# Kernel optimization log

Measured on AMD Instinct MI355X. Metric: run time of the kernel, lower is better.

The kernel has to match this reference:

```python
import jax, jax.numpy as jnp
import numpy as np

DIM = 2048
MEM = 64
EPS = 1e-5


def setup_inputs() -> dict:
    key = jax.random.key(0)
    ks = jax.random.split(key, 6)
    x = jax.random.normal(ks[0], (8, 4096, DIM), dtype=jnp.float32)
    memory_slots = jax.random.normal(ks[1], (MEM, DIM), dtype=jnp.float32) * 0.02
    # memory_gate: Linear(dim -> memory_size)
    Wg = jax.random.normal(ks[2], (DIM, MEM), dtype=jnp.float32) / np.sqrt(DIM)
    bg = jnp.zeros((MEM,), dtype=jnp.float32)
    # memory_update: Linear(2*dim -> dim)
    Wu = jax.random.normal(ks[3], (2 * DIM, DIM), dtype=jnp.float32) / np.sqrt(2 * DIM)
    bu = jnp.zeros((DIM,), dtype=jnp.float32)
    gamma = jnp.ones((DIM,), dtype=jnp.float32)
    beta = jnp.zeros((DIM,), dtype=jnp.float32)
    return {"x": x, "memory_slots": memory_slots, "Wg": Wg, "bg": bg,
            "Wu": Wu, "bu": bu, "gamma": gamma, "beta": beta}


def _layer_norm(h, gamma, beta):
    mu = jnp.mean(h, axis=-1, keepdims=True)
    var = jnp.mean(jnp.square(h - mu), axis=-1, keepdims=True)
    return (h - mu) * jax.lax.rsqrt(var + EPS) * gamma + beta


def reference(x, memory_slots, Wg, bg, Wu, bu, gamma, beta):
    # gates: [B, S, M]
    memory_gates = jax.nn.sigmoid(jnp.einsum('bsd,dm->bsm', x, Wg) + bg)
    # retrieval: [B, S, D]
    memory_retrieved = jnp.einsum('bsm,md->bsd', memory_gates, memory_slots)
    combined = jnp.concatenate([x, memory_retrieved], axis=-1)  # [B, S, 2D]
    memory_enhanced = jnp.einsum('bse,ed->bsd', combined, Wu) + bu
    return _layer_norm(memory_enhanced, gamma, beta)
```

## Files before the change

kernel.cpp:

```cpp
#include <hip/hip_runtime.h>
#include <hip/hip_bf16.h>

typedef __bf16 bf16x8 __attribute__((ext_vector_type(8)));
typedef float f32x4 __attribute__((ext_vector_type(4)));
typedef float f32x16 __attribute__((ext_vector_type(16)));
typedef unsigned short u16;
typedef u16 u16x8 __attribute__((ext_vector_type(8)));

#define DIM 2048
#define MEM 64
#define KC 2112
#define MTOK 32768
#define BK 32
#define NT (KC/BK)

__device__ __forceinline__ u16 f2bf(float f) {
  union { float f; unsigned u; } v; v.f = f;
  unsigned r = v.u + 0x7FFF + ((v.u >> 16) & 1);
  return (u16)(r >> 16);
}
__device__ __forceinline__ float bf2f(u16 u) {
  union { unsigned u; float f; } v; v.u = ((unsigned)u) << 16; return v.f;
}

#define GLDS16(g, l) __builtin_amdgcn_global_load_lds( \
    (const __attribute__((address_space(1))) void*)(g), \
    (__attribute__((address_space(3))) void*)(l), 16, 0, 0)

__global__ __launch_bounds__(256) void prep_wu1(const float* __restrict__ Wu,
                                                u16* __restrict__ WcatT) {
  __shared__ float tile[64][65];
  int bk = blockIdx.x & 31;
  int bn = blockIdx.x >> 5;
  int tx = threadIdx.x & 63, g = threadIdx.x >> 6;
#pragma unroll
  for (int i = 0; i < 16; ++i)
    tile[g + i*4][tx] = Wu[(size_t)(bk*64 + g + i*4)*DIM + bn*64 + tx];
  __syncthreads();
#pragma unroll
  for (int i = 0; i < 16; ++i) {
    int n = bn*64 + g + i*4;
    WcatT[(size_t)n*KC + bk*64 + tx] = f2bf(tile[tx][g + i*4]);
  }
}

__global__ __launch_bounds__(256) void prep_m2a(const float* __restrict__ ms,
                                                const float* __restrict__ Wu,
                                                float* __restrict__ M2p) {
  int n  = blockIdx.x*256 + threadIdx.x;
  int mg = blockIdx.y;
  int kc = blockIdx.z;
  const float* w2 = Wu + (size_t)DIM*DIM + n;
  const float* m0 = ms + (size_t)(mg*4+0)*DIM;
  const float* m1 = ms + (size_t)(mg*4+1)*DIM;
  const float* m2 = ms + (size_t)(mg*4+2)*DIM;
  const float* m3 = ms + (size_t)(mg*4+3)*DIM;
  float a0=0.f, a1=0.f, a2=0.f, a3=0.f;
  int d0 = kc*256;
  for (int d = d0; d < d0+256; ++d) {
    float w = w2[(size_t)d*DIM];
    a0 += m0[d]*w; a1 += m1[d]*w; a2 += m2[d]*w; a3 += m3[d]*w;
  }
  M2p[((size_t)kc*64 + mg*4 + 0)*2048 + n] = a0;
  M2p[((size_t)kc*64 + mg*4 + 1)*2048 + n] = a1;
  M2p[((size_t)kc*64 + mg*4 + 2)*2048 + n] = a2;
  M2p[((size_t)kc*64 + mg*4 + 3)*2048 + n] = a3;
}

__global__ __launch_bounds__(256) void prep_m2b(const float* __restrict__ M2p,
                                                u16* __restrict__ WcatT) {
  int i = blockIdx.x*256 + threadIdx.x;
  float s = 0.f;
#pragma unroll
  for (int kc = 0; kc < 8; ++kc) s += M2p[(size_t)kc*131072 + i];
  int m = i >> 11, n = i & 2047;
  WcatT[(size_t)n*KC + DIM + m] = f2bf(s);
}

__global__ __launch_bounds__(256) void prep_wg(const float* __restrict__ Wg,
                                               u16* __restrict__ WgT) {
  __shared__ float tile[64][65];
  int k0 = blockIdx.x * 64;
  int tx = threadIdx.x & 63, g = threadIdx.x >> 6;
#pragma unroll
  for (int i = 0; i < 16; ++i)
    tile[g + i*4][tx] = Wg[(size_t)(k0 + g + i*4)*MEM + tx];
  __syncthreads();
#pragma unroll
  for (int i = 0; i < 16; ++i) {
    int m = g + i*4;
    WgT[(size_t)m*DIM + k0 + tx] = f2bf(tile[tx][m]);
  }
}

__global__ __launch_bounds__(256) void conv_gates(const float* __restrict__ x,
                                                  const u16* __restrict__ WgT,
                                                  const float* __restrict__ bg,
                                                  u16* __restrict__ Acat) {
  __shared__ u16 As[64*32];
  __shared__ u16 Bs[64*32];
  const int brow = blockIdx.x;
  const int tid = threadIdx.x;
  const int w = tid >> 6, l = tid & 63;
  const int wm = w >> 1, wn = w & 1;
  const int lrow = l & 15, lk = l >> 4;

  const int r  = tid >> 2;
  const int cb = (tid & 3) * 8;
  const float* xp = x + (size_t)(brow*64 + r)*DIM + cb;
  u16* aout = Acat + (size_t)(brow*64 + r)*KC + cb;

  f32x4 acc[2][2] = {};
  const bf16x8* Al = reinterpret_cast<const bf16x8*>(As);
  const bf16x8* Bl = reinterpret_cast<const bf16x8*>(Bs);
  const int abase = (wm*32 + lrow)*4 + lk;
  const int bbase = (wn*32 + lrow)*4 + lk;

  float4 v0 = *reinterpret_cast<const float4*>(xp);
  float4 v1 = *reinterpret_cast<const float4*>(xp + 4);

  for (int k0 = 0; k0 < DIM; k0 += 32) {
    const u16* bgp = WgT + (size_t)(tid>>2)*DIM + k0 + (tid&3)*8;
    GLDS16(bgp, ((u16*)Bs) + tid*8);
    u16x8 o;
    o[0]=f2bf(v0.x); o[1]=f2bf(v0.y); o[2]=f2bf(v0.z); o[3]=f2bf(v0.w);
    o[4]=f2bf(v1.x); o[5]=f2bf(v1.y); o[6]=f2bf(v1.z); o[7]=f2bf(v1.w);
    const bool more = (k0 + 32 < DIM);
    if (more) {
      v0 = *reinterpret_cast<const float4*>(xp + k0 + 32);
      v1 = *reinterpret_cast<const float4*>(xp + k0 + 36);
    }
    __builtin_amdgcn_s_barrier();
    *reinterpret_cast<u16x8*>(As + tid*8) = o;
    *reinterpret_cast<u16x8*>(aout + k0) = o;
    if (more) { asm volatile("s_waitcnt vmcnt(3) lgkmcnt(0)" ::: "memory"); }
    else      { asm volatile("s_waitcnt vmcnt(1) lgkmcnt(0)" ::: "memory"); }
    __builtin_amdgcn_sched_barrier(0);
    __builtin_amdgcn_s_barrier();
    bf16x8 a0v = Al[abase], a1v = Al[abase + 64];
    bf16x8 b0v = Bl[bbase], b1v = Bl[bbase + 64];
    acc[0][0] = __builtin_amdgcn_mfma_f32_16x16x32_bf16(a0v, b0v, acc[0][0], 0, 0, 0);
    acc[0][1] = __builtin_amdgcn_mfma_f32_16x16x32_bf16(a0v, b1v, acc[0][1], 0, 0, 0);
    acc[1][0] = __builtin_amdgcn_mfma_f32_16x16x32_bf16(a1v, b0v, acc[1][0], 0, 0, 0);
    acc[1][1] = __builtin_amdgcn_mfma_f32_16x16x32_bf16(a1v, b1v, acc[1][1], 0, 0, 0);
  }

#pragma unroll
  for (int fn = 0; fn < 2; ++fn) {
    int c = wn*32 + fn*16 + lrow;
    float b = bg[c];
#pragma unroll
    for (int fm = 0; fm < 2; ++fm)
#pragma unroll
      for (int rg = 0; rg < 4; ++rg) {
        int t = brow*64 + wm*32 + fm*16 + lk*4 + rg;
        float logit = acc[fm][fn][rg] + b;
        float gv = 1.0f / (1.0f + __expf(-logit));
        Acat[(size_t)t*KC + DIM + c] = f2bf(gv);
      }
  }
}

__global__ __launch_bounds__(512, 2) void gemm_main8(const u16* __restrict__ A,
                                                     const u16* __restrict__ Bt,
                                                     const float* __restrict__ bu,
                                                     float* __restrict__ Hf,
                                                     u16* __restrict__ Hb) {
  __shared__ u16 AsB[4*8192];
  __shared__ u16 BsB[4*8192];

  const int bid = blockIdx.x;
  const int wg  = (bid & 7) * (int)(gridDim.x >> 3) + (bid >> 3);
  const int brow = wg >> 3;
  const int bcol = wg & 7;
  const int tid = threadIdx.x;
  const int w = tid >> 6, l = tid & 63;
  const int wm = w >> 2, wn = w & 3;
  const int l31 = l & 31, lr5 = l >> 5;

  const int xor5  = ((tid >> 5) & 1) << 5;
  const int kelem = (((tid & 3) * 16) ^ xor5) >> 1;
  const int rowst = tid >> 2;
  const u16* Asrc0 = A  + (size_t)(brow*256 + rowst)*KC + kelem;
  const u16* Asrc1 = A  + (size_t)(brow*256 + 128 + rowst)*KC + kelem;
  const u16* Bsrc0 = Bt + (size_t)(bcol*256 + rowst)*KC + kelem;
  const u16* Bsrc1 = Bt + (size_t)(bcol*256 + 128 + rowst)*KC + kelem;
  const int p0 = tid*16, p1 = 8192 + tid*16;
  char* AsC = (char*)AsB;
  char* BsC = (char*)BsB;

  int aoff[4][2], boff[2][2];
#pragma unroll
  for (int rf = 0; rf < 4; ++rf)
#pragma unroll
    for (int ks = 0; ks < 2; ++ks) {
      int row = wm*128 + rf*32 + l31;
      int lg  = row*64 + ks*32 + lr5*16;
      aoff[rf][ks] = lg ^ (((row >> 3) & 1) << 5);
    }
#pragma unroll
  for (int cf = 0; cf < 2; ++cf)
#pragma unroll
    for (int ks = 0; ks < 2; ++ks) {
      int row = wn*64 + cf*32 + l31;
      int lg  = row*64 + ks*32 + lr5*16;
      boff[cf][ks] = lg ^ (((row >> 3) & 1) << 5);
    }

  f32x16 acc[4][2] = {};

#define STAGE_A(kt) { const int bb_ = ((kt)&3)*16384; \
    GLDS16(Asrc0 + (size_t)(kt)*BK, AsC + bb_ + p0); \
    GLDS16(Asrc1 + (size_t)(kt)*BK, AsC + bb_ + p1); }
#define STAGE_B(kt) { const int bb_ = ((kt)&3)*16384; \
    GLDS16(Bsrc0 + (size_t)(kt)*BK, BsC + bb_ + p0); \
    GLDS16(Bsrc1 + (size_t)(kt)*BK, BsC + bb_ + p1); }
#define MFMA32(av, bv, c) __builtin_amdgcn_mfma_f32_32x32x16_bf16(av, bv, c, 0, 0, 0)

  STAGE_A(0); STAGE_B(0);
  STAGE_A(1); STAGE_B(1);
  STAGE_A(2); STAGE_B(2);
  asm volatile("s_waitcnt vmcnt(8)" ::: "memory");
  __builtin_amdgcn_sched_barrier(0);
  __builtin_amdgcn_s_barrier();
  __builtin_amdgcn_sched_barrier(0);

#pragma unroll 1
  for (int t = 0; t < NT; ++t) {
    const char* Ab = AsC + (t & 3) * 16384;
    const char* Bb = BsC + (t & 3) * 16384;

    bf16x8 a0 = *(const bf16x8*)(Ab + aoff[0][0]);
    bf16x8 a1 = *(const bf16x8*)(Ab + aoff[1][0]);
    bf16x8 a2 = *(const bf16x8*)(Ab + aoff[2][0]);
    bf16x8 a3 = *(const bf16x8*)(Ab + aoff[3][0]);
    bf16x8 b0 = *(const bf16x8*)(Bb + boff[0][0]);
    bf16x8 b1 = *(const bf16x8*)(Bb + boff[1][0]);
    if (t + 3 < NT) STAGE_A(t + 3);
    __builtin_amdgcn_s_setprio(1);
    acc[0][0] = MFMA32(a0, b0, acc[0][0]);
    acc[0][1] = MFMA32(a0, b1, acc[0][1]);
    acc[1][0] = MFMA32(a1, b0, acc[1][0]);
    acc[1][1] = MFMA32(a1, b1, acc[1][1]);
    acc[2][0] = MFMA32(a2, b0, acc[2][0]);
    acc[2][1] = MFMA32(a2, b1, acc[2][1]);
    acc[3][0] = MFMA32(a3, b0, acc[3][0]);
    acc[3][1] = MFMA32(a3, b1, acc[3][1]);
    __builtin_amdgcn_s_setprio(0);

    bf16x8 a4 = *(const bf16x8*)(Ab + aoff[0][1]);
    bf16x8 a5 = *(const bf16x8*)(Ab + aoff[1][1]);
    bf16x8 a6 = *(const bf16x8*)(Ab + aoff[2][1]);
    bf16x8 a7 = *(const bf16x8*)(Ab + aoff[3][1]);
    bf16x8 b2 = *(const bf16x8*)(Bb + boff[0][1]);
    bf16x8 b3 = *(const bf16x8*)(Bb + boff[1][1]);
    if (t + 3 < NT) STAGE_B(t + 3);
    __builtin_amdgcn_s_setprio(1);
    acc[0][0] = MFMA32(a4, b2, acc[0][0]);
    acc[0][1] = MFMA32(a4, b3, acc[0][1]);
    acc[1][0] = MFMA32(a5, b2, acc[1][0]);
    acc[1][1] = MFMA32(a5, b3, acc[1][1]);
    acc[2][0] = MFMA32(a6, b2, acc[2][0]);
    acc[2][1] = MFMA32(a6, b3, acc[2][1]);
    acc[3][0] = MFMA32(a7, b2, acc[3][0]);
    acc[3][1] = MFMA32(a7, b3, acc[3][1]);
    __builtin_amdgcn_s_setprio(0);

    if (t <= NT-4)      { asm volatile("s_waitcnt vmcnt(8)" ::: "memory"); }
    else if (t == NT-3) { asm volatile("s_waitcnt vmcnt(4)" ::: "memory"); }
    else                { asm volatile("s_waitcnt vmcnt(0)" ::: "memory"); }
    __builtin_amdgcn_sched_barrier(0);
    __builtin_amdgcn_s_barrier();
    __builtin_amdgcn_sched_barrier(0);
  }
#undef STAGE_A
#undef STAGE_B
#undef MFMA32

  const int orow = brow*256 + wm*128;
  const int ocol = bcol*256 + wn*64;
  if (Hb) {
#pragma unroll
    for (int cf = 0; cf < 2; ++cf) {
      const int c = ocol + cf*32 + l31;
      const float bias = bu[c];
#pragma unroll
      for (int rf = 0; rf < 4; ++rf) {
        const int br = orow + rf*32 + 4*lr5;
#pragma unroll
        for (int reg = 0; reg < 16; ++reg) {
          const int row = br + (reg & 3) + 8*(reg >> 2);
          Hb[(size_t)row*DIM + c] = f2bf(acc[rf][cf][reg] + bias);
        }
      }
    }
  } else {
#pragma unroll
    for (int cf = 0; cf < 2; ++cf) {
      const int c = ocol + cf*32 + l31;
      const float bias = bu[c];
#pragma unroll
      for (int rf = 0; rf < 4; ++rf) {
        const int br = orow + rf*32 + 4*lr5;
#pragma unroll
        for (int reg = 0; reg < 16; ++reg) {
          const int row = br + (reg & 3) + 8*(reg >> 2);
          Hf[(size_t)row*DIM + c] = acc[rf][cf][reg] + bias;
        }
      }
    }
  }
}

__global__ __launch_bounds__(256) void ln_b(const u16* __restrict__ Hb,
                                            float* __restrict__ out,
                                            const float* __restrict__ gamma,
                                            const float* __restrict__ beta) {
  const int tid = threadIdx.x;
  const int c0 = tid*8;
  const int w = tid >> 6;
  __shared__ float ss[4], ss2[4];
  float g8[8], be8[8];
#pragma unroll
  for (int j = 0; j < 8; ++j) { g8[j] = gamma[c0+j]; be8[j] = beta[c0+j]; }

#pragma unroll
  for (int rr = 0; rr < 2; ++rr) {
    const int row = blockIdx.x*2 + rr;
    const u16* h = Hb + (size_t)row*DIM;
    u16x8 hv = *reinterpret_cast<const u16x8*>(h + c0);
    float v[8];
#pragma unroll
    for (int j = 0; j < 8; ++j) v[j] = bf2f(hv[j]);
    float s = 0.f, s2 = 0.f;
#pragma unroll
    for (int j = 0; j < 8; ++j) { s += v[j]; s2 += v[j]*v[j]; }
#pragma unroll
    for (int o = 32; o >= 1; o >>= 1) { s += __shfl_xor(s, o); s2 += __shfl_xor(s2, o); }
    if ((tid & 63) == 0) { ss[w] = s; ss2[w] = s2; }
    __syncthreads();
    s  = ss[0]+ss[1]+ss[2]+ss[3];
    s2 = ss2[0]+ss2[1]+ss2[2]+ss2[3];
    __syncthreads();
    float mu  = s * (1.0f/DIM);
    float var = s2 * (1.0f/DIM) - mu*mu;
    float rs  = rsqrtf(var + 1e-5f);
    float o8[8];
#pragma unroll
    for (int j = 0; j < 8; ++j) o8[j] = (v[j]-mu)*rs*g8[j] + be8[j];
    float4 oa = {o8[0],o8[1],o8[2],o8[3]}, ob = {o8[4],o8[5],o8[6],o8[7]};
    float* op = out + (size_t)row*DIM;
    reinterpret_cast<float4*>(op)[tid*2]   = oa;
    reinterpret_cast<float4*>(op)[tid*2+1] = ob;
  }
}

__global__ __launch_bounds__(256) void ln_inplace(float* __restrict__ H,
                                                  const float* __restrict__ gamma,
                                                  const float* __restrict__ beta) {
  int row = blockIdx.x;
  float* h = H + (size_t)row*DIM;
  int tid = threadIdx.x;
  float4 a = reinterpret_cast<const float4*>(h)[tid*2];
  float4 b = reinterpret_cast<const float4*>(h)[tid*2+1];
  float v[8] = {a.x,a.y,a.z,a.w,b.x,b.y,b.z,b.w};
  float s = 0.f, s2 = 0.f;
#pragma unroll
  for (int j = 0; j < 8; ++j) { s += v[j]; s2 += v[j]*v[j]; }
#pragma unroll
  for (int o = 32; o >= 1; o >>= 1) { s += __shfl_xor(s, o); s2 += __shfl_xor(s2, o); }
  __shared__ float ss[4], ss2[4];
  int w = tid >> 6;
  if ((tid & 63) == 0) { ss[w] = s; ss2[w] = s2; }
  __syncthreads();
  s  = ss[0]+ss[1]+ss[2]+ss[3];
  s2 = ss2[0]+ss2[1]+ss2[2]+ss2[3];
  float mu  = s * (1.0f/DIM);
  float var = s2 * (1.0f/DIM) - mu*mu;
  float rs  = rsqrtf(var + 1e-5f);
  int c0 = tid*8;
  float o8[8];
#pragma unroll
  for (int j = 0; j < 8; ++j) o8[j] = (v[j]-mu)*rs*gamma[c0+j] + beta[c0+j];
  float4 oa = {o8[0],o8[1],o8[2],o8[3]}, ob = {o8[4],o8[5],o8[6],o8[7]};
  reinterpret_cast<float4*>(h)[tid*2]   = oa;
  reinterpret_cast<float4*>(h)[tid*2+1] = ob;
}

extern "C" void kernel_launch(void* const* d_in, const int* in_sizes, int n_in,
                              void* d_out, int out_size, void* d_ws, size_t ws_size,
                              hipStream_t stream) {
  const float* x     = (const float*)d_in[0];
  const float* ms    = (const float*)d_in[1];
  const float* Wg    = (const float*)d_in[2];
  const float* bg    = (const float*)d_in[3];
  const float* Wu    = (const float*)d_in[4];
  const float* bu    = (const float*)d_in[5];
  const float* gamma = (const float*)d_in[6];
  const float* beta  = (const float*)d_in[7];
  float* out = (float*)d_out;

  char* wsp = (char*)d_ws;
  const size_t offAcat  = 0;
  const size_t offWcatT = offAcat  + (size_t)MTOK*KC*2;
  const size_t offWgT   = offWcatT + (size_t)DIM*KC*2;
  const size_t offHb    = offWgT   + (size_t)MEM*DIM*2;
  const size_t needHb   = offHb + (size_t)MTOK*DIM*2;

  u16* Acat  = (u16*)(wsp + offAcat);
  u16* WcatT = (u16*)(wsp + offWcatT);
  u16* WgT   = (u16*)(wsp + offWgT);
  float* M2p = (float*)wsp;
  u16* Hb    = (ws_size >= needHb) ? (u16*)(wsp + offHb) : nullptr;

  prep_m2a<<<dim3(8,16,8), 256, 0, stream>>>(ms, Wu, M2p);
  prep_m2b<<<512, 256, 0, stream>>>(M2p, WcatT);
  prep_wu1<<<1024, 256, 0, stream>>>(Wu, WcatT);
  prep_wg<<<32, 256, 0, stream>>>(Wg, WgT);
  conv_gates<<<512, 256, 0, stream>>>(x, WgT, bg, Acat);
  gemm_main8<<<1024, 512, 0, stream>>>(Acat, WcatT, bu, out, Hb);
  if (Hb) ln_b<<<16384, 256, 0, stream>>>(Hb, out, gamma, beta);
  else    ln_inplace<<<32768, 256, 0, stream>>>(out, gamma, beta);
}
```

Before: 533.2 us.

## Rework main GEMM to 16x16x32 MFMA with BK=64 double-buffered split-K pipeline

The main bf16 GEMM now uses 16x16x32 MFMA tiles instead of 32x32x16. Each iteration consumes 64 K-elements from a double buffer, split into two 32-wide halves, instead of 32 K-elements from a four-stage ring. Global-to-LDS staging of the next tile is interleaved with the MFMA groups using extra barriers and finer vmcnt waits, and the LDS swizzle and epilogue indexing change to match the new fragment layout. The aim is better overlap of loads with compute and fewer loop iterations. The cost is more barriers per iteration and a shallower prefetch depth.

```diff
diff --git a/kernel.cpp b/kernel.cpp
--- a/kernel.cpp
+++ b/kernel.cpp
@@ -3,7 +3,6 @@
 
 typedef __bf16 bf16x8 __attribute__((ext_vector_type(8)));
 typedef float f32x4 __attribute__((ext_vector_type(4)));
-typedef float f32x16 __attribute__((ext_vector_type(16)));
 typedef unsigned short u16;
 typedef u16 u16x8 __attribute__((ext_vector_type(8)));
 
@@ -11,8 +10,7 @@
 #define MEM 64
 #define KC 2112
 #define MTOK 32768
-#define BK 32
-#define NT (KC/BK)
+#define NT64 33
 
 __device__ __forceinline__ u16 f2bf(float f) {
   union { float f; unsigned u; } v; v.f = f;
@@ -166,8 +164,8 @@
                                                      const float* __restrict__ bu,
                                                      float* __restrict__ Hf,
                                                      u16* __restrict__ Hb) {
-  __shared__ u16 AsB[4*8192];
-  __shared__ u16 BsB[4*8192];
+  __shared__ u16 AsB[2*2*8192];
+  __shared__ u16 BsB[2*2*8192];
 
   const int bid = blockIdx.x;
   const int wg  = (bid & 7) * (int)(gridDim.x >> 3) + (bid >> 3);
@@ -176,137 +174,164 @@
   const int tid = threadIdx.x;
   const int w = tid >> 6, l = tid & 63;
   const int wm = w >> 2, wn = w & 3;
-  const int l31 = l & 31, lr5 = l >> 5;
-
-  const int xor5  = ((tid >> 5) & 1) << 5;
-  const int kelem = (((tid & 3) * 16) ^ xor5) >> 1;
-  const int rowst = tid >> 2;
-  const u16* Asrc0 = A  + (size_t)(brow*256 + rowst)*KC + kelem;
-  const u16* Asrc1 = A  + (size_t)(brow*256 + 128 + rowst)*KC + kelem;
-  const u16* Bsrc0 = Bt + (size_t)(bcol*256 + rowst)*KC + kelem;
-  const u16* Bsrc1 = Bt + (size_t)(bcol*256 + 128 + rowst)*KC + kelem;
-  const int p0 = tid*16, p1 = 8192 + tid*16;
+  const int l15 = l & 15, lk = l >> 4;
+
   char* AsC = (char*)AsB;
   char* BsC = (char*)BsB;
 
-  int aoff[4][2], boff[2][2];
-#pragma unroll
-  for (int rf = 0; rf < 4; ++rf)
-#pragma unroll
-    for (int ks = 0; ks < 2; ++ks) {
-      int row = wm*128 + rf*32 + l31;
-      int lg  = row*64 + ks*32 + lr5*16;
-      aoff[rf][ks] = lg ^ (((row >> 3) & 1) << 5);
-    }
-#pragma unroll
-  for (int cf = 0; cf < 2; ++cf)
-#pragma unroll
-    for (int ks = 0; ks < 2; ++ks) {
-      int row = wn*64 + cf*32 + l31;
-      int lg  = row*64 + ks*32 + lr5*16;
-      boff[cf][ks] = lg ^ (((row >> 3) & 1) << 5);
-    }
-
-  f32x16 acc[4][2] = {};
-
-#define STAGE_A(kt) { const int bb_ = ((kt)&3)*16384; \
-    GLDS16(Asrc0 + (size_t)(kt)*BK, AsC + bb_ + p0); \
-    GLDS16(Asrc1 + (size_t)(kt)*BK, AsC + bb_ + p1); }
-#define STAGE_B(kt) { const int bb_ = ((kt)&3)*16384; \
-    GLDS16(Bsrc0 + (size_t)(kt)*BK, BsC + bb_ + p0); \
-    GLDS16(Bsrc1 + (size_t)(kt)*BK, BsC + bb_ + p1); }
-#define MFMA32(av, bv, c) __builtin_amdgcn_mfma_f32_32x32x16_bf16(av, bv, c, 0, 0, 0)
-
-  STAGE_A(0); STAGE_B(0);
-  STAGE_A(1); STAGE_B(1);
-  STAGE_A(2); STAGE_B(2);
-  asm volatile("s_waitcnt vmcnt(8)" ::: "memory");
+  const int po0 = tid*16, po1 = 8192 + tid*16;
+  const int lo0 = po0 ^ (((po0 >> 9) & 1) << 5);
+  const int lo1 = po1 ^ (((po1 >> 9) & 1) << 5);
+  const int r0 = lo0 >> 6, k0e = (lo0 & 63) >> 1;
+  const int r1 = lo1 >> 6, k1e = (lo1 & 63) >> 1;
+  const u16* Ag0 = A  + (size_t)(brow*256 + r0)*KC + k0e;
+  const u16* Ag1 = A  + (size_t)(brow*256 + r1)*KC + k1e;
+  const u16* Bg0 = Bt + (size_t)(bcol*256 + r0)*KC + k0e;
+  const u16* Bg1 = Bt + (size_t)(bcol*256 + r1)*KC + k1e;
+
+  int aoff[8], boff[4];
+#pragma unroll
+  for (int rf = 0; rf < 8; ++rf) {
+    int row = wm*128 + rf*16 + l15;
+    int lg  = row*64 + lk*16;
+    aoff[rf] = lg ^ (((lg >> 9) & 1) << 5);
+  }
+#pragma unroll
+  for (int cf = 0; cf < 4; ++cf) {
+    int row = wn*64 + cf*16 + l15;
+    int lg  = row*64 + lk*16;
+    boff[cf] = lg ^ (((lg >> 9) & 1) << 5);
+  }
+
+  f32x4 acc[8][4] = {};
+
+#define STAGE_A_KH(kt, kh) { char* d_ = AsC + ((kt)&1)*32768 + (kh)*16384; \
+    GLDS16(Ag0 + (size_t)(kt)*64 + (kh)*32, d_ + po0); \
+    GLDS16(Ag1 + (size_t)(kt)*64 + (kh)*32, d_ + po1); }
+#define STAGE_B_KH(kt, kh) { char* d_ = BsC + ((kt)&1)*32768 + (kh)*16384; \
+    GLDS16(Bg0 + (size_t)(kt)*64 + (kh)*32, d_ + po0); \
+    GLDS16(Bg1 + (size_t)(kt)*64 + (kh)*32, d_ + po1); }
+#define MFMA16(av, bv, c) __builtin_amdgcn_mfma_f32_16x16x32_bf16(av, bv, c, 0, 0, 0)
+
+  STAGE_A_KH(0, 0); STAGE_B_KH(0, 0);
+  STAGE_A_KH(0, 1); STAGE_B_KH(0, 1);
+  asm volatile("s_waitcnt vmcnt(0)" ::: "memory");
   __builtin_amdgcn_sched_barrier(0);
   __builtin_amdgcn_s_barrier();
   __builtin_amdgcn_sched_barrier(0);
 
 #pragma unroll 1
-  for (int t = 0; t < NT; ++t) {
-    const char* Ab = AsC + (t & 3) * 16384;
-    const char* Bb = BsC + (t & 3) * 16384;
-
-    bf16x8 a0 = *(const bf16x8*)(Ab + aoff[0][0]);
-    bf16x8 a1 = *(const bf16x8*)(Ab + aoff[1][0]);
-    bf16x8 a2 = *(const bf16x8*)(Ab + aoff[2][0]);
-    bf16x8 a3 = *(const bf16x8*)(Ab + aoff[3][0]);
-    bf16x8 b0 = *(const bf16x8*)(Bb + boff[0][0]);
-    bf16x8 b1 = *(const bf16x8*)(Bb + boff[1][0]);
-    if (t + 3 < NT) STAGE_A(t + 3);
-    __builtin_amdgcn_s_setprio(1);
-    acc[0][0] = MFMA32(a0, b0, acc[0][0]);
-    acc[0][1] = MFMA32(a0, b1, acc[0][1]);
-    acc[1][0] = MFMA32(a1, b0, acc[1][0]);
-    acc[1][1] = MFMA32(a1, b1, acc[1][1]);
-    acc[2][0] = MFMA32(a2, b0, acc[2][0]);
-    acc[2][1] = MFMA32(a2, b1, acc[2][1]);
-    acc[3][0] = MFMA32(a3, b0, acc[3][0]);
-    acc[3][1] = MFMA32(a3, b1, acc[3][1]);
-    __builtin_amdgcn_s_setprio(0);
-
-    bf16x8 a4 = *(const bf16x8*)(Ab + aoff[0][1]);
-    bf16x8 a5 = *(const bf16x8*)(Ab + aoff[1][1]);
-    bf16x8 a6 = *(const bf16x8*)(Ab + aoff[2][1]);
-    bf16x8 a7 = *(const bf16x8*)(Ab + aoff[3][1]);
-    bf16x8 b2 = *(const bf16x8*)(Bb + boff[0][1]);
-    bf16x8 b3 = *(const bf16x8*)(Bb + boff[1][1]);
-    if (t + 3 < NT) STAGE_B(t + 3);
-    __builtin_amdgcn_s_setprio(1);
-    acc[0][0] = MFMA32(a4, b2, acc[0][0]);
-    acc[0][1] = MFMA32(a4, b3, acc[0][1]);
-    acc[1][0] = MFMA32(a5, b2, acc[1][0]);
-    acc[1][1] = MFMA32(a5, b3, acc[1][1]);
-    acc[2][0] = MFMA32(a6, b2, acc[2][0]);
-    acc[2][1] = MFMA32(a6, b3, acc[2][1]);
-    acc[3][0] = MFMA32(a7, b2, acc[3][0]);
-    acc[3][1] = MFMA32(a7, b3, acc[3][1]);
-    __builtin_amdgcn_s_setprio(0);
-
-    if (t <= NT-4)      { asm volatile("s_waitcnt vmcnt(8)" ::: "memory"); }
-    else if (t == NT-3) { asm volatile("s_waitcnt vmcnt(4)" ::: "memory"); }
-    else                { asm volatile("s_waitcnt vmcnt(0)" ::: "memory"); }
-    __builtin_amdgcn_sched_barrier(0);
-    __builtin_amdgcn_s_barrier();
-    __builtin_amdgcn_sched_barrier(0);
-  }
-#undef STAGE_A
-#undef STAGE_B
-#undef MFMA32
-
-  const int orow = brow*256 + wm*128;
-  const int ocol = bcol*256 + wn*64;
+  for (int t = 0; t < NT64; ++t) {
+    const bool more = (t + 1 < NT64);
+    bf16x8 a0, a1, a2, a3, a4, a5, a6, a7, b0, b1, b2, b3;
+
+#pragma unroll
+    for (int ks = 0; ks < 2; ++ks) {
+      const char* Ah = AsC + (t & 1)*32768 + ks*16384;
+      const char* Bh = BsC + (t & 1)*32768 + ks*16384;
+
+      a0 = *(const bf16x8*)(Ah + aoff[0]);
+      a1 = *(const bf16x8*)(Ah + aoff[1]);
+      a2 = *(const bf16x8*)(Ah + aoff[2]);
+      a3 = *(const bf16x8*)(Ah + aoff[3]);
+      a4 = *(const bf16x8*)(Ah + aoff[4]);
+      a5 = *(const bf16x8*)(Ah + aoff[5]);
+      a6 = *(const bf16x8*)(Ah + aoff[6]);
+      a7 = *(const bf16x8*)(Ah + aoff[7]);
+      b0 = *(const bf16x8*)(Bh + boff[0]);
+      b1 = *(const bf16x8*)(Bh + boff[1]);
+      if (more) STAGE_A_KH(t + 1, ks);
+      __builtin_amdgcn_s_barrier();
+      asm volatile("s_waitcnt lgkmcnt(0)" ::: "memory");
+      __builtin_amdgcn_sched_barrier(0);
+      __builtin_amdgcn_s_setprio(1);
+      acc[0][0] = MFMA16(a0, b0, acc[0][0]);
+      acc[0][1] = MFMA16(a0, b1, acc[0][1]);
+      acc[1][0] = MFMA16(a1, b0, acc[1][0]);
+      acc[1][1] = MFMA16(a1, b1, acc[1][1]);
+      acc[2][0] = MFMA16(a2, b0, acc[2][0]);
+      acc[2][1] = MFMA16(a2, b1, acc[2][1]);
+      acc[3][0] = MFMA16(a3, b0, acc[3][0]);
+      acc[3][1] = MFMA16(a3, b1, acc[3][1]);
+      acc[4][0] = MFMA16(a4, b0, acc[4][0]);
+      acc[4][1] = MFMA16(a4, b1, acc[4][1]);
+      acc[5][0] = MFMA16(a5, b0, acc[5][0]);
+      acc[5][1] = MFMA16(a5, b1, acc[5][1]);
+      acc[6][0] = MFMA16(a6, b0, acc[6][0]);
+      acc[6][1] = MFMA16(a6, b1, acc[6][1]);
+      acc[7][0] = MFMA16(a7, b0, acc[7][0]);
+      acc[7][1] = MFMA16(a7, b1, acc[7][1]);
+      __builtin_amdgcn_s_setprio(0);
+      if (ks == 0) { if (more) { asm volatile("s_waitcnt vmcnt(6)" ::: "memory"); }
+                     else      { asm volatile("s_waitcnt vmcnt(2)" ::: "memory"); } }
+      else         { if (more) { asm volatile("s_waitcnt vmcnt(6)" ::: "memory"); }
+                     else      { asm volatile("s_waitcnt vmcnt(0)" ::: "memory"); } }
+      __builtin_amdgcn_sched_barrier(0);
+      __builtin_amdgcn_s_barrier();
+      __builtin_amdgcn_sched_barrier(0);
+
+      b2 = *(const bf16x8*)(Bh + boff[2]);
+      b3 = *(const bf16x8*)(Bh + boff[3]);
+      if (more) STAGE_B_KH(t + 1, ks);
+      __builtin_amdgcn_s_barrier();
+      asm volatile("s_waitcnt lgkmcnt(0)" ::: "memory");
+      __builtin_amdgcn_sched_barrier(0);
+      __builtin_amdgcn_s_setprio(1);
+      acc[0][2] = MFMA16(a0, b2, acc[0][2]);
+      acc[0][3] = MFMA16(a0, b3, acc[0][3]);
+      acc[1][2] = MFMA16(a1, b2, acc[1][2]);
+      acc[1][3] = MFMA16(a1, b3, acc[1][3]);
+      acc[2][2] = MFMA16(a2, b2, acc[2][2]);
+      acc[2][3] = MFMA16(a2, b3, acc[2][3]);
+      acc[3][2] = MFMA16(a3, b2, acc[3][2]);
+      acc[3][3] = MFMA16(a3, b3, acc[3][3]);
+      acc[4][2] = MFMA16(a4, b2, acc[4][2]);
+      acc[4][3] = MFMA16(a4, b3, acc[4][3]);
+      acc[5][2] = MFMA16(a5, b2, acc[5][2]);
+      acc[5][3] = MFMA16(a5, b3, acc[5][3]);
+      acc[6][2] = MFMA16(a6, b2, acc[6][2]);
+      acc[6][3] = MFMA16(a6, b3, acc[6][3]);
+      acc[7][2] = MFMA16(a7, b2, acc[7][2]);
+      acc[7][3] = MFMA16(a7, b3, acc[7][3]);
+      __builtin_amdgcn_s_setprio(0);
+      if (ks == 0) { if (more) { asm volatile("s_waitcnt vmcnt(6)" ::: "memory"); }
+                     else      { asm volatile("s_waitcnt vmcnt(0)" ::: "memory"); } }
+      else if (more) { asm volatile("s_waitcnt vmcnt(4)" ::: "memory"); }
+      __builtin_amdgcn_sched_barrier(0);
+      __builtin_amdgcn_s_barrier();
+      __builtin_amdgcn_sched_barrier(0);
+    }
+  }
+#undef STAGE_A_KH
+#undef STAGE_B_KH
+#undef MFMA16
+
+  const int orow = brow*256 + wm*128 + lk*4;
+  const int ocol = bcol*256 + wn*64 + l15;
   if (Hb) {
 #pragma unroll
-    for (int cf = 0; cf < 2; ++cf) {
-      const int c = ocol + cf*32 + l31;
+    for (int cf = 0; cf < 4; ++cf) {
+      const int c = ocol + cf*16;
       const float bias = bu[c];
 #pragma unroll
-      for (int rf = 0; rf < 4; ++rf) {
-        const int br = orow + rf*32 + 4*lr5;
-#pragma unroll
-        for (int reg = 0; reg < 16; ++reg) {
-          const int row = br + (reg & 3) + 8*(reg >> 2);
-          Hb[(size_t)row*DIM + c] = f2bf(acc[rf][cf][reg] + bias);
-        }
+      for (int rf = 0; rf < 8; ++rf) {
+        const int rr = orow + rf*16;
+#pragma unroll
+        for (int r = 0; r < 4; ++r)
+          Hb[(size_t)(rr + r)*DIM + c] = f2bf(acc[rf][cf][r] + bias);
       }
     }
   } else {
 #pragma unroll
-    for (int cf = 0; cf < 2; ++cf) {
-      const int c = ocol + cf*32 + l31;
+    for (int cf = 0; cf < 4; ++cf) {
+      const int c = ocol + cf*16;
       const float bias = bu[c];
 #pragma unroll
-      for (int rf = 0; rf < 4; ++rf) {
-        const int br = orow + rf*32 + 4*lr5;
-#pragma unroll
-        for (int reg = 0; reg < 16; ++reg) {
-          const int row = br + (reg & 3) + 8*(reg >> 2);
-          Hf[(size_t)row*DIM + c] = acc[rf][cf][reg] + bias;
-        }
+      for (int rf = 0; rf < 8; ++rf) {
+        const int rr = orow + rf*16;
+#pragma unroll
+        for (int r = 0; r < 4; ++r)
+          Hf[(size_t)(rr + r)*DIM + c] = acc[rf][cf][r] + bias;
       }
     }
   }
```

New measurement: 534.7 us. About the same (+0.3%).
